# Performance work log

Measured on AMD Instinct MI355X. Metric: run time of the kernel, lower is better.

## Reference

```python
import jax, jax.numpy as jnp
import numpy as np


def _grid_sample_bilinear(img, grid):
    # img: [B,C,H,W]; grid: [B,Hg,Wg,2] normalized to [-1,1] (x,y), align_corners=False,
    # zero padding (torch F.grid_sample defaults).
    B, C, H, W = img.shape
    Hg, Wg = grid.shape[1], grid.shape[2]
    gx, gy = grid[..., 0], grid[..., 1]
    ix = (gx + 1.0) * (W * 0.5) - 0.5
    iy = (gy + 1.0) * (H * 0.5) - 0.5
    ix0 = jnp.floor(ix)
    iy0 = jnp.floor(iy)
    tx = (ix - ix0).reshape(B, 1, -1)
    ty = (iy - iy0).reshape(B, 1, -1)
    img_flat = img.reshape(B, C, H * W)

    def corner(xi, yi):
        valid = ((xi >= 0) & (xi < W) & (yi >= 0) & (yi < H)).reshape(B, 1, -1)
        xc = jnp.clip(xi, 0, W - 1).astype(jnp.int32)
        yc = jnp.clip(yi, 0, H - 1).astype(jnp.int32)
        idx = (yc * W + xc).reshape(B, -1)                      # [B, Hg*Wg]
        vals = jax.vmap(lambda f, i: f[:, i])(img_flat, idx)    # [B, C, Hg*Wg]
        return vals * valid

    v00 = corner(ix0, iy0)
    v01 = corner(ix0 + 1, iy0)
    v10 = corner(ix0, iy0 + 1)
    v11 = corner(ix0 + 1, iy0 + 1)
    out = (v00 * (1 - tx) * (1 - ty) + v01 * tx * (1 - ty)
           + v10 * (1 - tx) * ty + v11 * tx * ty)
    return out.reshape(B, C, Hg, Wg)


def setup_inputs() -> dict:
    key = jax.random.key(0)
    ks = jax.random.split(key, 8)
    B, C, RHO, WP = 32, 384, 25, 256
    HC, WC = 64, 64
    D = 2 * C  # 768, channels after polar/cart concat
    std = 0.02
    return {
        "polar_feat": jax.random.normal(ks[0], (B, C, RHO, WP), jnp.float32),
        "cart_feat": jax.random.normal(ks[1], (B, C, HC, WC), jnp.float32),
        "grid": jax.random.uniform(ks[2], (B, RHO, WP, 2), jnp.float32, -1.0, 1.0),
        "W1_0": jax.random.normal(ks[3], (D, 40), jnp.float32) * std,
        "b1_0": jnp.zeros((40,), jnp.float32),
        "W2_0": jax.random.normal(ks[4], (40, 1), jnp.float32) * std,
        "b2_0": jnp.zeros((1,), jnp.float32),
        "W1s": jax.random.normal(ks[5], (24, D + 1, 40), jnp.float32) * std,
        "b1s": jnp.zeros((24, 40), jnp.float32),
        "W2s": jax.random.normal(ks[6], (24, 40, 1), jnp.float32) * std,
        "b2s": jnp.zeros((24, 1), jnp.float32),
    }


def reference(polar_feat, cart_feat, grid, W1_0, b1_0, W2_0, b2_0, W1s, b1s, W2s, b2s):
    # Polar grid-sample fusion of cartesian features onto the polar grid.
    fe_cart_p = _grid_sample_bilinear(cart_feat, grid)              # [B,C,25,Wp]
    fe_cat_p = jnp.concatenate([polar_feat, fe_cart_p], axis=1)     # [B,768,25,Wp]
    # AdaptiveAvgPool2d((None,1)): mean over width.
    fe = jnp.mean(fe_cat_p, axis=3)                                 # [B,768,25]

    feats = jnp.transpose(fe, (2, 0, 1))                            # [25,B,768]
    gelu = lambda x: jax.nn.gelu(x, approximate=False)

    # Head 0: no recurrent input.
    h0 = gelu(feats[0] @ W1_0 + b1_0)
    out0 = h0 @ W2_0 + b2_0                                         # [B,1]

    # Heads 1..24: concat previous scalar output before first linear (fully_local=False).
    def step(out_prev, xs):
        feat, W1, b1, W2, b2 = xs
        x = jnp.concatenate([feat, out_prev], axis=-1)              # [B,769]
        h = gelu(x @ W1 + b1)
        o = h @ W2 + b2                                             # [B,1]
        return o, o

    _, outs = jax.lax.scan(step, out0, (feats[1:], W1s, b1s, W2s, b2s))
    out = jnp.concatenate([out0[None], outs], axis=0)               # [25,B,1]
    out = jnp.transpose(out[:, :, 0], (1, 0))                       # [B,25]
    return jnp.clip(out, 0.0, jnp.pi)
```

## Files before the change

### kernel.cpp

```cpp
#include <hip/hip_runtime.h>
#include <math.h>

#define B_    32
#define C_    384
#define RHO_  25
#define WP_   256
#define PIX_  4096
#define D_    768
#define HID_  40
#define NROWS (B_*C_*RHO_)
#define PCHUNK 4
#define FE_N (RHO_*B_*D_)
#define CARTBLK 768
#define MAINBLK 1536
#define PNW (768*4)

__device__ __forceinline__ float gelu_exact(float x) {
    return 0.5f * x * (1.f + erff(x * 0.70710678118654752f));
}

__device__ __forceinline__ void gl_lds16(const float* g, float* l) {
    __builtin_amdgcn_global_load_lds((const __attribute__((address_space(1))) void*)g,
                                     (__attribute__((address_space(3))) void*)l, 16, 0, 0);
}

__global__ __launch_bounds__(256) void prep_kernel(const float* __restrict__ grid,
        const float* __restrict__ W1_0, const float* __restrict__ W1s,
        float* __restrict__ bins, float* __restrict__ W1T, float* __restrict__ fe) {
    __shared__ float lb[PIX_];
    int tid = threadIdx.x;
    if (blockIdx.x < B_ * RHO_) {
        for (int i = tid; i < PIX_ / 4; i += 256) ((float4*)lb)[i] = make_float4(0.f, 0.f, 0.f, 0.f);
        __syncthreads();
        int pt = blockIdx.x * WP_ + tid;
        float2 g = ((const float2*)grid)[pt];
        float ix = (g.x + 1.f) * 32.f - 0.5f;
        float iy = (g.y + 1.f) * 32.f - 0.5f;
        float x0f = floorf(ix), y0f = floorf(iy);
        float fx = ix - x0f, fy = iy - y0f;
        int x0 = (int)x0f, y0 = (int)y0f;
        const float s = 1.f / 256.f;
        if ((unsigned)x0 < 64u) {
            if ((unsigned)y0 < 64u)       atomicAdd(&lb[y0 * 64 + x0],       (1.f - fx) * (1.f - fy) * s);
            if ((unsigned)(y0 + 1) < 64u) atomicAdd(&lb[(y0 + 1) * 64 + x0], (1.f - fx) * fy * s);
        }
        if ((unsigned)(x0 + 1) < 64u) {
            if ((unsigned)y0 < 64u)       atomicAdd(&lb[y0 * 64 + x0 + 1],       fx * (1.f - fy) * s);
            if ((unsigned)(y0 + 1) < 64u) atomicAdd(&lb[(y0 + 1) * 64 + x0 + 1], fx * fy * s);
        }
        __syncthreads();
        float4* dst = (float4*)(bins + (size_t)blockIdx.x * PIX_);
        for (int i = tid; i < PIX_ / 4; i += 256) dst[i] = ((float4*)lb)[i];
    } else if (blockIdx.x < B_ * RHO_ + 25) {
        int i = blockIdx.x - B_ * RHO_;
        const float* src = (i == 0) ? W1_0 : (W1s + (size_t)(i - 1) * 769 * HID_);
        float* dst = W1T + (size_t)i * HID_ * D_;
        for (int idx = tid; idx < HID_ * D_; idx += 256) {
            int j = idx / D_, c = idx % D_;
            dst[idx] = src[c * HID_ + j];
        }
    } else {
        int z = blockIdx.x - (B_ * RHO_ + 25);
        float4* f4 = (float4*)fe;
        int per = FE_N / 4 / 50;
        for (int i = tid; i < per; i += 256)
            f4[z * per + i] = make_float4(0.f, 0.f, 0.f, 0.f);
    }
}

__global__ __launch_bounds__(256) void main_kernel(const float* __restrict__ polar,
        const float* __restrict__ cart, const float* __restrict__ bins,
        float* __restrict__ fe) {
    __shared__ float smem[12288];
    const int BUF = 6144;
    int tid = threadIdx.x;
    int lane = tid & 63, w = tid >> 6;

    if ((blockIdx.x & 1) == 0) {
        int idx = blockIdx.x >> 1;
        int b  = idx / (6 * PCHUNK);
        int ct = (idx / PCHUNK) % 6;
        int pc = idx % PCHUNK;
        int c0 = ct * 64;
        int h = lane >> 4;
        int c = tid & 15, q = tid >> 4;
        const float* binb  = bins + (size_t)b * RHO_ * PIX_ + pc * 1024;
        const float* cartb = cart + ((size_t)b * C_ + c0) * PIX_ + pc * 1024;

        const float* gX[4]; int uXo[4];
        #pragma unroll
        for (int k = 0; k < 4; ++k) {
            int u = w + 4 * k;
            int row = 4 * u + h;
            gX[k] = cartb + (size_t)row * PIX_ + (((lane & 15) ^ (row & 15)) << 2);
            uXo[k] = u << 8;
        }
        const float* gW[2]; int uWo[2];
        #pragma unroll
        for (int k = 0; k < 2; ++k) {
            int u = w + 4 * k;
            gW[k] = binb + (size_t)(4 * u + h) * PIX_ + ((lane & 15) << 2);
            uWo[k] = 4096 + (u << 8);
        }

        float acc[4][25];
        #pragma unroll
        for (int jj = 0; jj < 4; ++jj)
            #pragma unroll
            for (int r = 0; r < 25; ++r) acc[jj][r] = 0.f;

        #pragma unroll
        for (int k = 0; k < 4; ++k) gl_lds16(gX[k], smem + uXo[k]);
        #pragma unroll
        for (int k = 0; k < 2; ++k) gl_lds16(gW[k], smem + uWo[k]);

        for (int t = 0; t < 16; ++t) {
            int cbase = (t & 1) * BUF;
            int nbase = cbase ^ BUF;
            if (t < 15) {
                int p0 = (t + 1) << 6;
                #pragma unroll
                for (int k = 0; k < 4; ++k) gl_lds16(gX[k] + p0, smem + nbase + uXo[k]);
                #pragma unroll
                for (int k = 0; k < 2; ++k) gl_lds16(gW[k] + p0, smem + nbase + uWo[k]);
                asm volatile("s_waitcnt vmcnt(6)" ::: "memory");
            } else {
                asm volatile("s_waitcnt vmcnt(0)" ::: "memory");
            }
            __builtin_amdgcn_sched_barrier(0);
            __builtin_amdgcn_s_barrier();
            const float* Xb = smem + cbase;
            const float* Wb = smem + cbase + 4096;
            int sx = (q ^ c) << 2;
            float4 x0 = *(const float4*)(Xb + ((c     ) << 6) + sx);
            float4 x1 = *(const float4*)(Xb + ((c + 16) << 6) + sx);
            float4 x2 = *(const float4*)(Xb + ((c + 32) << 6) + sx);
            float4 x3 = *(const float4*)(Xb + ((c + 48) << 6) + sx);
            #pragma unroll
            for (int r = 0; r < 25; ++r) {
                float4 wv = *(const float4*)(Wb + (r << 6) + (q << 2));
                acc[0][r] += x0.x * wv.x + x0.y * wv.y + x0.z * wv.z + x0.w * wv.w;
                acc[1][r] += x1.x * wv.x + x1.y * wv.y + x1.z * wv.z + x1.w * wv.w;
                acc[2][r] += x2.x * wv.x + x2.y * wv.y + x2.z * wv.z + x2.w * wv.w;
                acc[3][r] += x3.x * wv.x + x3.y * wv.y + x3.z * wv.z + x3.w * wv.w;
            }
            __builtin_amdgcn_s_barrier();
        }

        #pragma unroll
        for (int jj = 0; jj < 4; ++jj)
            #pragma unroll
            for (int r = 0; r < 25; ++r) {
                acc[jj][r] += __shfl_xor(acc[jj][r], 16, 64);
                acc[jj][r] += __shfl_xor(acc[jj][r], 32, 64);
            }
        if (lane < 16) {
            #pragma unroll
            for (int jj = 0; jj < 4; ++jj)
                #pragma unroll
                for (int r = 0; r < 25; ++r)
                    smem[((w * 4 + jj) * 16 + c) * 25 + r] = acc[jj][r];
        }
        __syncthreads();
        for (int oi = tid; oi < 1600; oi += 256) {
            int cc = oi / 25, r = oi % 25;
            int jj = cc >> 4, cl = cc & 15;
            float ssum = 0.f;
            #pragma unroll
            for (int ww = 0; ww < 4; ++ww)
                ssum += smem[((ww * 4 + jj) * 16 + cl) * 25 + r];
            atomicAdd(&fe[((size_t)(r * B_ + b)) * D_ + 384 + c0 + cc], ssum);
        }
    } else {
        int wid = (blockIdx.x >> 1) * 4 + w;
        for (int it = 0; it < 25; ++it) {
            int r0 = wid + it * 4 * PNW;
            float s[4];
            #pragma unroll
            for (int k = 0; k < 4; ++k) {
                float4 v = ((const float4*)(polar + (size_t)(r0 + k * PNW) * WP_))[lane];
                s[k] = v.x + v.y + v.z + v.w;
            }
            #pragma unroll
            for (int m = 32; m >= 1; m >>= 1) {
                #pragma unroll
                for (int k = 0; k < 4; ++k) s[k] += __shfl_xor(s[k], m, 64);
            }
            if (lane == 0) {
                #pragma unroll
                for (int k = 0; k < 4; ++k) {
                    int r = r0 + k * PNW;
                    int rho = r % RHO_, cch = (r / RHO_) % C_, bb = r / (RHO_ * C_);
                    fe[((size_t)(rho * B_ + bb)) * D_ + cch] = s[k] * (1.f / 256.f);
                }
            }
        }
    }
}

__global__ __launch_bounds__(256) void mlp_pre_kernel(const float* __restrict__ fe,
        const float* __restrict__ W1T, const float* __restrict__ b1_0,
        const float* __restrict__ b1s, float* __restrict__ G) {
    int lane = threadIdx.x & 63;
    int trip = blockIdx.x * 4 + (threadIdx.x >> 6);
    int jh = trip & 1;
    int pair = trip >> 1;
    int i = pair >> 5, b = pair & 31;
    const float4* f4p = (const float4*)(fe + (size_t)(i * B_ + b) * D_);
    float4 f0 = f4p[lane], f1 = f4p[lane + 64], f2 = f4p[lane + 128];
    int j0 = jh * 20;
    #pragma unroll 2
    for (int j = j0; j < j0 + 20; ++j) {
        const float4* w4p = (const float4*)(W1T + ((size_t)i * HID_ + j) * D_);
        float4 w0 = w4p[lane], w1 = w4p[lane + 64], w2 = w4p[lane + 128];
        float s = f0.x*w0.x + f0.y*w0.y + f0.z*w0.z + f0.w*w0.w
                + f1.x*w1.x + f1.y*w1.y + f1.z*w1.z + f1.w*w1.w
                + f2.x*w2.x + f2.y*w2.y + f2.z*w2.z + f2.w*w2.w;
        #pragma unroll
        for (int m = 32; m >= 1; m >>= 1) s += __shfl_xor(s, m, 64);
        if (lane == 0) {
            float bias = (i == 0) ? b1_0[j] : b1s[(i - 1) * HID_ + j];
            G[(size_t)(i * B_ + b) * HID_ + j] = s + bias;
        }
    }
}

__global__ __launch_bounds__(64) void mlp_seq_kernel(const float* __restrict__ G,
        const float* __restrict__ W1s, const float* __restrict__ W2_0,
        const float* __restrict__ b2_0, const float* __restrict__ W2s,
        const float* __restrict__ b2s, float* __restrict__ out) {
    int lane = threadIdx.x;
    int j2 = lane & 31, b = blockIdx.x * 2 + (lane >> 5);
    bool hi = (j2 < 8);
    float g1[25], g2[25], wl1[25], wl2[25], w2a[25], w2b[25], bsc[25];
    #pragma unroll
    for (int i = 0; i < 25; ++i) {
        g1[i] = G[(size_t)(i * B_ + b) * HID_ + j2];
        g2[i] = hi ? G[(size_t)(i * B_ + b) * HID_ + 32 + j2] : 0.f;
    }
    wl1[0] = 0.f; wl2[0] = 0.f;
    w2a[0] = W2_0[j2]; w2b[0] = hi ? W2_0[32 + j2] : 0.f; bsc[0] = b2_0[0];
    #pragma unroll
    for (int i = 1; i < 25; ++i) {
        size_t base = ((size_t)(i - 1) * 769 + 768) * HID_;
        wl1[i] = W1s[base + j2];
        wl2[i] = hi ? W1s[base + 32 + j2] : 0.f;
        w2a[i] = W2s[(i - 1) * HID_ + j2];
        w2b[i] = hi ? W2s[(i - 1) * HID_ + 32 + j2] : 0.f;
        bsc[i] = b2s[i - 1];
    }
    float op = 0.f;
    #pragma unroll
    for (int i = 0; i < 25; ++i) {
        float x1 = g1[i] + op * wl1[i];
        float x2 = g2[i] + op * wl2[i];
        float p = gelu_exact(x1) * w2a[i] + gelu_exact(x2) * w2b[i];
        #pragma unroll
        for (int m = 16; m >= 1; m >>= 1) p += __shfl_xor(p, m, 64);
        float o = p + bsc[i];
        op = o;
        if (j2 == 0) out[b * 25 + i] = fminf(fmaxf(o, 0.f), 3.14159265358979323846f);
    }
}

extern "C" void kernel_launch(void* const* d_in, const int* in_sizes, int n_in,
                              void* d_out, int out_size, void* d_ws, size_t ws_size,
                              hipStream_t stream) {
    const float* polar = (const float*)d_in[0];
    const float* cart  = (const float*)d_in[1];
    const float* grid  = (const float*)d_in[2];
    const float* W1_0  = (const float*)d_in[3];
    const float* b1_0  = (const float*)d_in[4];
    const float* W2_0  = (const float*)d_in[5];
    const float* b2_0  = (const float*)d_in[6];
    const float* W1s   = (const float*)d_in[7];
    const float* b1s   = (const float*)d_in[8];
    const float* W2s   = (const float*)d_in[9];
    const float* b2s   = (const float*)d_in[10];
    float* out = (float*)d_out;

    float* bins = (float*)d_ws;
    float* fe   = bins + (size_t)(B_ * RHO_ + 8) * PIX_;
    float* G    = fe + (size_t)FE_N;
    float* W1T  = G + (size_t)RHO_ * B_ * HID_;

    prep_kernel<<<B_ * RHO_ + 25 + 50, 256, 0, stream>>>(grid, W1_0, W1s, bins, W1T, fe);
    main_kernel<<<MAINBLK, 256, 0, stream>>>(polar, cart, bins, fe);
    mlp_pre_kernel<<<(RHO_ * B_ * 2) / 4, 256, 0, stream>>>(fe, W1T, b1_0, b1s, G);
    mlp_seq_kernel<<<B_ / 2, 64, 0, stream>>>(G, W1s, W2_0, b2_0, W2s, b2s, out);
}
```

Baseline: 213.7 us.

## Halve cart channel tile and rebalance polar/cart block interleaving

The cart GEMM blocks now handle 32 channels instead of 64, which doubles the block count, halves LDS use and accumulator registers, and should allow more resident waves. Blocks are interleaved in groups of 8 cart and 8 polar blocks instead of alternating one by one. Each polar wave now reduces 50 contiguous rows, two at a time, instead of strided rows four at a time. The trade-off is that each cart tile is reused over fewer channels, so the bins tile is loaded twice as often, and there are twice as many atomic launches.

New measurement: 242.8 us. +13.6%, slower.

```diff
diff --git a/kernel.cpp b/kernel.cpp
--- a/kernel.cpp
+++ b/kernel.cpp
@@ -11,9 +11,8 @@
 #define NROWS (B_*C_*RHO_)
 #define PCHUNK 4
 #define FE_N (RHO_*B_*D_)
-#define CARTBLK 768
-#define MAINBLK 1536
-#define PNW (768*4)
+#define MAINBLK 3072
+#define PROWS 50
 
 __device__ __forceinline__ float gelu_exact(float x) {
     return 0.5f * x * (1.f + erff(x * 0.70710678118654752f));
@@ -71,48 +70,43 @@
 __global__ __launch_bounds__(256) void main_kernel(const float* __restrict__ polar,
         const float* __restrict__ cart, const float* __restrict__ bins,
         float* __restrict__ fe) {
-    __shared__ float smem[12288];
-    const int BUF = 6144;
+    __shared__ float smem[8192];
+    const int BUF = 4096;
     int tid = threadIdx.x;
     int lane = tid & 63, w = tid >> 6;
-
-    if ((blockIdx.x & 1) == 0) {
-        int idx = blockIdx.x >> 1;
-        int b  = idx / (6 * PCHUNK);
-        int ct = (idx / PCHUNK) % 6;
-        int pc = idx % PCHUNK;
-        int c0 = ct * 64;
+    int bid = blockIdx.x;
+    int idx = ((bid >> 4) << 3) + (bid & 7);
+
+    if (((bid >> 3) & 1) == 0) {
+        int b  = idx / 48;
+        int ct = (idx / 4) % 12;
+        int pc = idx & 3;
+        int c0 = ct * 32;
         int h = lane >> 4;
         int c = tid & 15, q = tid >> 4;
         const float* binb  = bins + (size_t)b * RHO_ * PIX_ + pc * 1024;
         const float* cartb = cart + ((size_t)b * C_ + c0) * PIX_ + pc * 1024;
 
-        const float* gX[4]; int uXo[4];
-        #pragma unroll
-        for (int k = 0; k < 4; ++k) {
+        const float* gX[2]; int uXo[2];
+        const float* gW[2]; int uWo[2];
+        #pragma unroll
+        for (int k = 0; k < 2; ++k) {
             int u = w + 4 * k;
             int row = 4 * u + h;
             gX[k] = cartb + (size_t)row * PIX_ + (((lane & 15) ^ (row & 15)) << 2);
             uXo[k] = u << 8;
-        }
-        const float* gW[2]; int uWo[2];
-        #pragma unroll
-        for (int k = 0; k < 2; ++k) {
-            int u = w + 4 * k;
-            gW[k] = binb + (size_t)(4 * u + h) * PIX_ + ((lane & 15) << 2);
-            uWo[k] = 4096 + (u << 8);
-        }
-
-        float acc[4][25];
-        #pragma unroll
-        for (int jj = 0; jj < 4; ++jj)
+            gW[k] = binb + (size_t)row * PIX_ + ((lane & 15) << 2);
+            uWo[k] = 2048 + (u << 8);
+        }
+
+        float acc[2][25];
+        #pragma unroll
+        for (int jj = 0; jj < 2; ++jj)
             #pragma unroll
             for (int r = 0; r < 25; ++r) acc[jj][r] = 0.f;
 
         #pragma unroll
-        for (int k = 0; k < 4; ++k) gl_lds16(gX[k], smem + uXo[k]);
-        #pragma unroll
-        for (int k = 0; k < 2; ++k) gl_lds16(gW[k], smem + uWo[k]);
+        for (int k = 0; k < 2; ++k) { gl_lds16(gX[k], smem + uXo[k]); gl_lds16(gW[k], smem + uWo[k]); }
 
         for (int t = 0; t < 16; ++t) {
             int cbase = (t & 1) * BUF;
@@ -120,35 +114,32 @@
             if (t < 15) {
                 int p0 = (t + 1) << 6;
                 #pragma unroll
-                for (int k = 0; k < 4; ++k) gl_lds16(gX[k] + p0, smem + nbase + uXo[k]);
-                #pragma unroll
-                for (int k = 0; k < 2; ++k) gl_lds16(gW[k] + p0, smem + nbase + uWo[k]);
-                asm volatile("s_waitcnt vmcnt(6)" ::: "memory");
+                for (int k = 0; k < 2; ++k) {
+                    gl_lds16(gX[k] + p0, smem + nbase + uXo[k]);
+                    gl_lds16(gW[k] + p0, smem + nbase + uWo[k]);
+                }
+                asm volatile("s_waitcnt vmcnt(4)" ::: "memory");
             } else {
                 asm volatile("s_waitcnt vmcnt(0)" ::: "memory");
             }
             __builtin_amdgcn_sched_barrier(0);
             __builtin_amdgcn_s_barrier();
             const float* Xb = smem + cbase;
-            const float* Wb = smem + cbase + 4096;
+            const float* Wb = smem + cbase + 2048;
             int sx = (q ^ c) << 2;
             float4 x0 = *(const float4*)(Xb + ((c     ) << 6) + sx);
             float4 x1 = *(const float4*)(Xb + ((c + 16) << 6) + sx);
-            float4 x2 = *(const float4*)(Xb + ((c + 32) << 6) + sx);
-            float4 x3 = *(const float4*)(Xb + ((c + 48) << 6) + sx);
             #pragma unroll
             for (int r = 0; r < 25; ++r) {
                 float4 wv = *(const float4*)(Wb + (r << 6) + (q << 2));
                 acc[0][r] += x0.x * wv.x + x0.y * wv.y + x0.z * wv.z + x0.w * wv.w;
                 acc[1][r] += x1.x * wv.x + x1.y * wv.y + x1.z * wv.z + x1.w * wv.w;
-                acc[2][r] += x2.x * wv.x + x2.y * wv.y + x2.z * wv.z + x2.w * wv.w;
-                acc[3][r] += x3.x * wv.x + x3.y * wv.y + x3.z * wv.z + x3.w * wv.w;
             }
             __builtin_amdgcn_s_barrier();
         }
 
         #pragma unroll
-        for (int jj = 0; jj < 4; ++jj)
+        for (int jj = 0; jj < 2; ++jj)
             #pragma unroll
             for (int r = 0; r < 25; ++r) {
                 acc[jj][r] += __shfl_xor(acc[jj][r], 16, 64);
@@ -156,43 +147,38 @@
             }
         if (lane < 16) {
             #pragma unroll
-            for (int jj = 0; jj < 4; ++jj)
+            for (int jj = 0; jj < 2; ++jj)
                 #pragma unroll
                 for (int r = 0; r < 25; ++r)
-                    smem[((w * 4 + jj) * 16 + c) * 25 + r] = acc[jj][r];
+                    smem[((w * 2 + jj) * 16 + c) * 25 + r] = acc[jj][r];
         }
         __syncthreads();
-        for (int oi = tid; oi < 1600; oi += 256) {
+        for (int oi = tid; oi < 800; oi += 256) {
             int cc = oi / 25, r = oi % 25;
             int jj = cc >> 4, cl = cc & 15;
             float ssum = 0.f;
             #pragma unroll
             for (int ww = 0; ww < 4; ++ww)
-                ssum += smem[((ww * 4 + jj) * 16 + cl) * 25 + r];
+                ssum += smem[((ww * 2 + jj) * 16 + cl) * 25 + r];
             atomicAdd(&fe[((size_t)(r * B_ + b)) * D_ + 384 + c0 + cc], ssum);
         }
     } else {
-        int wid = (blockIdx.x >> 1) * 4 + w;
-        for (int it = 0; it < 25; ++it) {
-            int r0 = wid + it * 4 * PNW;
-            float s[4];
-            #pragma unroll
-            for (int k = 0; k < 4; ++k) {
-                float4 v = ((const float4*)(polar + (size_t)(r0 + k * PNW) * WP_))[lane];
-                s[k] = v.x + v.y + v.z + v.w;
-            }
-            #pragma unroll
-            for (int m = 32; m >= 1; m >>= 1) {
-                #pragma unroll
-                for (int k = 0; k < 4; ++k) s[k] += __shfl_xor(s[k], m, 64);
-            }
+        int wid = idx * 4 + w;
+        int r0 = wid * PROWS;
+        for (int it = 0; it < PROWS / 2; ++it) {
+            int r = r0 + it * 2;
+            float4 v0 = ((const float4*)(polar + (size_t)r * WP_))[lane];
+            float4 v1 = ((const float4*)(polar + (size_t)(r + 1) * WP_))[lane];
+            float sa = v0.x + v0.y + v0.z + v0.w;
+            float sb = v1.x + v1.y + v1.z + v1.w;
+            #pragma unroll
+            for (int m = 32; m >= 1; m >>= 1) { sa += __shfl_xor(sa, m, 64); sb += __shfl_xor(sb, m, 64); }
             if (lane == 0) {
-                #pragma unroll
-                for (int k = 0; k < 4; ++k) {
-                    int r = r0 + k * PNW;
-                    int rho = r % RHO_, cch = (r / RHO_) % C_, bb = r / (RHO_ * C_);
-                    fe[((size_t)(rho * B_ + bb)) * D_ + cch] = s[k] * (1.f / 256.f);
-                }
+                int rho = r % RHO_, cch = (r / RHO_) % C_, bb = r / (RHO_ * C_);
+                fe[((size_t)(rho * B_ + bb)) * D_ + cch] = sa * (1.f / 256.f);
+                int r2 = r + 1;
+                int rho2 = r2 % RHO_, c2 = (r2 / RHO_) % C_, b2 = r2 / (RHO_ * C_);
+                fe[((size_t)(rho2 * B_ + b2)) * D_ + c2] = sb * (1.f / 256.f);
             }
         }
     }
```
